# Kernel optimization log

Hardware: AMD Instinct MI355X
Metric: run time of the kernel (lower is better)

Reference implementation:

```python
import jax, jax.numpy as jnp
import numpy as np

MUL0, MUL1 = 128, 64
DIM1 = MUL0 + 3 * MUL1          # 320 = dim of 128x0e + 64x1o
DIM2 = 4                        # 1x0e + 1x1o
WDIM, H = 16, 64
# per-instruction weight sizes (mul_in2 = 1), e3nn instruction order
N1 = MUL0 * MUL0                # (0e x 0e -> 0e)
N2 = MUL0 * MUL1                # (0e x 1o -> 1o)
N3 = MUL1 * MUL1                # (1o x 0e -> 1o)
N4 = MUL1 * MUL0                # (1o x 1o -> 0e)
WNUMEL = N1 + N2 + N3 + N4      # 36864
FAN = MUL0 + MUL1               # summed fan-in per output slice = 192
PW0 = float(np.sqrt(1.0 / FAN))         # path weight, component/element norm, l_out=0
PW1 = float(np.sqrt(3.0 / FAN))         # l_out=1 (alpha = 2l+1 = 3)
INV_SQRT3 = float(1.0 / np.sqrt(3.0))   # wigner_3j(1,1,0)/(0,1,1)/(1,0,1) entries
SQRT_K = float(1.0 / np.sqrt(FAN))      # tp_rescale correction (output divided by this)


def setup_inputs() -> dict:
    key = jax.random.key(0)
    ks = jax.random.split(key, 8)
    N = 4096

    def lin(k, fin, fout):
        k1, k2 = jax.random.split(k)
        lim = 1.0 / np.sqrt(fin)
        W = jax.random.uniform(k1, (fin, fout), minval=-lim, maxval=lim, dtype=jnp.float32)
        b = jax.random.uniform(k2, (fout,), minval=-lim, maxval=lim, dtype=jnp.float32)
        return W, b

    W0, b0 = lin(ks[3], WDIM, H)
    W1, b1 = lin(ks[4], H, H)
    W2, b2 = lin(ks[5], H, WNUMEL)
    return {
        "data_in1": jax.random.normal(ks[0], (N, DIM1), dtype=jnp.float32),
        "data_in2": jax.random.normal(ks[1], (N, DIM2), dtype=jnp.float32),
        "weight": jax.random.normal(ks[2], (N, WDIM), dtype=jnp.float32),
        "W0": W0, "b0": b0, "W1": W1, "b1": b1, "W2": W2, "b2": b2,
        "bias": jax.random.uniform(ks[6], (MUL0,), minval=-SQRT_K, maxval=SQRT_K, dtype=jnp.float32),
    }


def _forward(data_in1, data_in2, weight, W0, b0, W1, b1, W2, b2, bias):
    # weight-generating MLP: 16 -> 64 -> 64 -> weight_numel
    h = jax.nn.relu(weight @ W0 + b0)
    h = jax.nn.relu(h @ W1 + b1)
    w = h @ W2 + b2                                   # [N, WNUMEL] per-sample tp weights
    # split inputs into irrep blocks
    s1 = data_in1[:, :MUL0]                           # [N,128]  128x0e
    v1 = data_in1[:, MUL0:].reshape(-1, MUL1, 3)      # [N,64,3]  64x1o
    s2 = data_in2[:, 0]                               # [N]       1x0e
    v2 = data_in2[:, 1:4]                             # [N,3]     1x1o
    # per-instruction weight views (uvw with v=1 collapsed)
    Wa = w[:, :N1].reshape(-1, MUL0, MUL0)                   # 0e x 0e -> 0e
    Wb = w[:, N1:N1 + N2].reshape(-1, MUL0, MUL1)            # 0e x 1o -> 1o
    Wc = w[:, N1 + N2:N1 + N2 + N3].reshape(-1, MUL1, MUL1)  # 1o x 0e -> 1o
    Wd = w[:, N1 + N2 + N3:].reshape(-1, MUL1, MUL0)         # 1o x 1o -> 0e
    dot12 = jnp.einsum('eui,ei->eu', v1, v2)          # [N,64]
    # scalar (0e) output slice: paths Wa (w3j=1) and Wd (w3j = delta/sqrt(3))
    out0 = PW0 * (jnp.einsum('euw,eu->ew', Wa, s1) * s2[:, None]
                  + INV_SQRT3 * jnp.einsum('euw,eu->ew', Wd, dot12))
    # vector (1o) output slice: paths Wb and Wc (w3j = delta/sqrt(3))
    out1 = PW1 * INV_SQRT3 * (
        jnp.einsum('euw,eu->ew', Wb, s1)[:, :, None] * v2[:, None, :]
        + jnp.einsum('euw,eui->ewi', Wc, v1) * s2[:, None, None])
    out = jnp.concatenate([out0, out1.reshape(-1, 3 * MUL1)], axis=1)  # [N,320]
    out = out / SQRT_K                                # tp_rescale: divide by sqrt_k correction
    out = out.at[:, :MUL0].add(bias)                  # bias added on 0e slice only
    return out


def reference(data_in1, data_in2, weight, W0, b0, W1, b1, W2, b2, bias):
    return _forward(data_in1, data_in2, weight, W0, b0, W1, b1, W2, b2, bias)
```

## Files before the change

### kernel.cpp

```cpp
#include <hip/hip_runtime.h>
#include <hip/hip_bf16.h>

typedef __attribute__((ext_vector_type(8))) short short8;
typedef __attribute__((ext_vector_type(4))) float f32x4;
typedef __attribute__((ext_vector_type(4))) unsigned uint4v;

constexpr int N1 = 16384, N2 = 8192, N3 = 4096;
constexpr int WN = 36864;
constexpr float ISQ3 = 0.57735026918962576451f;

__device__ __forceinline__ unsigned short f2bf(float f) {
  unsigned u = __builtin_bit_cast(unsigned, f);
  u += 0x7fffu + ((u >> 16) & 1u);
  return (unsigned short)(u >> 16);
}

__device__ __forceinline__ unsigned pkbf(float a, float b) {
  unsigned r;
  asm("v_cvt_pk_bf16_f32 %0, %1, %2" : "=v"(r) : "v"(a), "v"(b));
  return r;
}

#define MFMA(a, b, c) __builtin_amdgcn_mfma_f32_16x16x32_bf16((a), (b), (c), 0, 0, 0)

#define CVT8(X0, X1, G) do { uint4v w_;                                       \
    w_[0] = pkbf(X0[0], X0[1]); w_[1] = pkbf(X0[2], X0[3]);                   \
    w_[2] = pkbf(X1[0], X1[1]); w_[3] = pkbf(X1[2], X1[3]);                   \
    G = __builtin_bit_cast(short8, w_); } while (0)

#define LOADH(EF, LO, HI) do {                                                \
    const float* hp_ = H + (size_t)(e0 + 16 * (EF) + nl) * 64 + grp * 8;      \
    f32x4 x0_ = *(const f32x4*)hp_,        x1_ = *(const f32x4*)(hp_ + 4);    \
    f32x4 x2_ = *(const f32x4*)(hp_ + 32), x3_ = *(const f32x4*)(hp_ + 36);   \
    CVT8(x0_, x1_, LO); CVT8(x2_, x3_, HI); } while (0)

__global__ __launch_bounds__(256)
void k_prep(const float* __restrict__ wgt, const float* __restrict__ W0,
            const float* __restrict__ b0, const float* __restrict__ W1,
            const float* __restrict__ b1, const float* __restrict__ W2,
            const float* __restrict__ d1, const float* __restrict__ d2,
            float* __restrict__ H, unsigned short* __restrict__ Bp,
            float* __restrict__ sBg, float* __restrict__ sDg,
            float* __restrict__ sCg, float* __restrict__ d2T) {
  __shared__ __align__(16) float shm[10400];
  const int bid = blockIdx.x;
  const int tid = threadIdx.x;

  if (bid < 288) {
    const int n0 = bid * 128;
#pragma unroll
    for (int q = 0; q < 8; ++q) {
      const int flat = tid + q * 256;
      const int row = flat >> 5, c4 = flat & 31;
      *(f32x4*)&shm[row * 132 + c4 * 4] =
          *(const f32x4*)(W2 + (size_t)row * WN + n0 + c4 * 4);
    }
    __syncthreads();
#pragma unroll
    for (int q = 0; q < 4; ++q) {
      const int p = tid + q * 256;
      const int ntl = p >> 7, kh = (p >> 6) & 1, lane2 = p & 63;
      const int k0 = kh * 32 + (lane2 >> 4) * 8;
      const int col = ntl * 16 + (lane2 & 15);
      short8 v;
#pragma unroll
      for (int qq = 0; qq < 8; ++qq) v[qq] = (short)f2bf(shm[(k0 + qq) * 132 + col]);
      *(short8*)(Bp + ((size_t)(n0 * 8 + p)) * 8) = v;
    }
  } else if (bid < 1312) {
    float* h0s = shm;
    const int r = tid >> 6, jj = tid & 63;
    const int e = (bid - 288) * 4 + r;
    float a = b0[jj];
#pragma unroll
    for (int i = 0; i < 16; ++i) a = fmaf(wgt[e * 16 + i], W0[i * 64 + jj], a);
    h0s[r * 64 + jj] = fmaxf(a, 0.f);
    __syncthreads();
    float a1 = b1[jj];
#pragma unroll
    for (int i = 0; i < 64; ++i) a1 = fmaf(h0s[r * 64 + i], W1[i * 64 + jj], a1);
    H[e * 64 + jj] = fmaxf(a1, 0.f);
  } else {
    float* d1s = shm;
    float* d2s = shm + 10272;
    const int e0 = (bid - 1312) * 32;
    for (int x = tid; x < 32 * 320; x += 256) {
      int e = x / 320, c = x % 320;
      d1s[e * 321 + c] = d1[(size_t)(e0 + e) * 320 + c];
    }
    if (tid < 128) d2s[tid] = d2[(size_t)e0 * 4 + tid];
    __syncthreads();
    const int e = tid & 31;
    const float s2 = d2s[e * 4 + 0];
    const float w1 = d2s[e * 4 + 1], w2 = d2s[e * 4 + 2], w3 = d2s[e * 4 + 3];
    for (int row = 128 + (tid >> 5); row < 516; row += 8) {
      float v; float* dst;
      if (row < 256)      { v = d1s[e * 321 + (row - 128)];            dst = sBg + (size_t)(row - 128) * 4096; }
      else if (row < 320) { int u = row - 256;
        v = ISQ3 * (d1s[e * 321 + 128 + 3 * u] * w1 + d1s[e * 321 + 129 + 3 * u] * w2 +
                    d1s[e * 321 + 130 + 3 * u] * w3);                  dst = sDg + (size_t)u * 4096; }
      else if (row < 512) { v = d1s[e * 321 + 128 + (row - 320)] * s2; dst = sCg + (size_t)(row - 320) * 4096; }
      else                { v = d2s[e * 4 + (row - 512)];              dst = d2T + (size_t)(row - 512) * 4096; }
      dst[e0 + e] = v;
    }
  }
}

__global__ __launch_bounds__(256, 3)
void k_main(const float* __restrict__ sBg, const float* __restrict__ sDg,
            const float* __restrict__ sCg, const float* __restrict__ d2T,
            const float* __restrict__ H, const unsigned short* __restrict__ Bp,
            const float* __restrict__ b2, const float* __restrict__ bias,
            float* __restrict__ out) {
  __shared__ __align__(16) float buf[8448];
  const int bid = blockIdx.x, tid = threadIdx.x;
  const int wid = tid >> 6, lane = tid & 63;
  const int nl = lane & 15, grp = lane >> 4;
  const short8* Bp8 = (const short8*)Bp;
  const f32x4 Zv = {0.f, 0.f, 0.f, 0.f};

  if (bid < 512) {
    const int j = bid & 7;
    const int e0 = (bid >> 3) * 64;
    short8 hL0, hH0, hL1, hH1, hL2, hH2, hL3, hH3;
    LOADH(0, hL0, hH0);
    LOADH(1, hL1, hH1);
    LOADH(2, hL2, hH2);
    LOADH(3, hL3, hH3);

    f32x4 aA0 = Zv, aA1 = Zv, aA2 = Zv, aA3 = Zv;
    f32x4 aD0 = Zv, aD1 = Zv, aD2 = Zv, aD3 = Zv;

    {
      const int u0 = wid * 32;
      const short8* pa = Bp8 + (size_t)(u0 * 8 + j) * 128 + lane;
      const float* sb = sBg + (size_t)u0 * 4096 + e0 + nl;
      const float* pb = b2 + (size_t)u0 * 128 + 16 * j + 4 * grp;
      short8 Fa[3], Fb[3]; f32x4 Bv[3];
      float S0[3], S1[3], S2[3], S3[3];
#pragma unroll
      for (int q = 0; q < 3; ++q) {
        Fa[q] = pa[0]; Fb[q] = pa[64];
        Bv[q] = *(const f32x4*)pb;
        S0[q] = sb[0]; S1[q] = sb[16]; S2[q] = sb[32]; S3[q] = sb[48];
        pa += 1024; sb += 4096; pb += 128;
      }
#pragma unroll
      for (int t = 0; t < 32; ++t) {
        const int s = t % 3;
        short8 f0 = Fa[s], f1 = Fb[s]; f32x4 b = Bv[s];
        float c0 = S0[s], c1 = S1[s], c2 = S2[s], c3 = S3[s];
        if (t < 29) {
          Fa[s] = pa[0]; Fb[s] = pa[64];
          Bv[s] = *(const f32x4*)pb;
          S0[s] = sb[0]; S1[s] = sb[16]; S2[s] = sb[32]; S3[s] = sb[48];
          pa += 1024; sb += 4096; pb += 128;
        }
        f32x4 tt;
        tt = MFMA(f0, hL0, b); tt = MFMA(f1, hH0, tt); aA0 += c0 * tt;
        tt = MFMA(f0, hL1, b); tt = MFMA(f1, hH1, tt); aA1 += c1 * tt;
        tt = MFMA(f0, hL2, b); tt = MFMA(f1, hH2, tt); aA2 += c2 * tt;
        tt = MFMA(f0, hL3, b); tt = MFMA(f1, hH3, tt); aA3 += c3 * tt;
      }
    }
    {
      const int u0 = wid * 16;
      const short8* pa = Bp8 + (size_t)(1792 + u0 * 8 + j) * 128 + lane;
      const float* sd = sDg + (size_t)u0 * 4096 + e0 + nl;
      const float* pb = b2 + (size_t)(N1 + N2 + N3) + (size_t)u0 * 128 + 16 * j + 4 * grp;
      short8 Fa[3], Fb[3]; f32x4 Bv[3];
      float S0[3], S1[3], S2[3], S3[3];
#pragma unroll
      for (int q = 0; q < 3; ++q) {
        Fa[q] = pa[0]; Fb[q] = pa[64];
        Bv[q] = *(const f32x4*)pb;
        S0[q] = sd[0]; S1[q] = sd[16]; S2[q] = sd[32]; S3[q] = sd[48];
        pa += 1024; sd += 4096; pb += 128;
      }
#pragma unroll
      for (int t = 0; t < 16; ++t) {
        const int s = t % 3;
        short8 f0 = Fa[s], f1 = Fb[s]; f32x4 b = Bv[s];
        float c0 = S0[s], c1 = S1[s], c2 = S2[s], c3 = S3[s];
        if (t < 13) {
          Fa[s] = pa[0]; Fb[s] = pa[64];
          Bv[s] = *(const f32x4*)pb;
          S0[s] = sd[0]; S1[s] = sd[16]; S2[s] = sd[32]; S3[s] = sd[48];
          pa += 1024; sd += 4096; pb += 128;
        }
        f32x4 tt;
        tt = MFMA(f0, hL0, b); tt = MFMA(f1, hH0, tt); aD0 += c0 * tt;
        tt = MFMA(f0, hL1, b); tt = MFMA(f1, hH1, tt); aD1 += c1 * tt;
        tt = MFMA(f0, hL2, b); tt = MFMA(f1, hH2, tt); aD2 += c2 * tt;
        tt = MFMA(f0, hL3, b); tt = MFMA(f1, hH3, tt); aD3 += c3 * tt;
      }
    }
    {
      float* bw = &buf[wid * 2112];
#pragma unroll
      for (int r = 0; r < 4; ++r) {
        bw[nl * 33 + grp * 4 + r]             = aA0[r];
        bw[(16 + nl) * 33 + grp * 4 + r]      = aA1[r];
        bw[(32 + nl) * 33 + grp * 4 + r]      = aA2[r];
        bw[(48 + nl) * 33 + grp * 4 + r]      = aA3[r];
        bw[nl * 33 + 16 + grp * 4 + r]        = aD0[r];
        bw[(16 + nl) * 33 + 16 + grp * 4 + r] = aD1[r];
        bw[(32 + nl) * 33 + 16 + grp * 4 + r] = aD2[r];
        bw[(48 + nl) * 33 + 16 + grp * 4 + r] = aD3[r];
      }
      __syncthreads();
#pragma unroll
      for (int it = 0; it < 4; ++it) {
        const int p = tid + it * 256;
        const int e = p >> 4, w = p & 15;
        float ta = buf[e * 33 + w] + buf[2112 + e * 33 + w] +
                   buf[4224 + e * 33 + w] + buf[6336 + e * 33 + w];
        float td = buf[e * 33 + 16 + w] + buf[2112 + e * 33 + 16 + w] +
                   buf[4224 + e * 33 + 16 + w] + buf[6336 + e * 33 + 16 + w];
        out[(size_t)(e0 + e) * 320 + 16 * j + w] = d2T[e0 + e] * ta + td + bias[16 * j + w];
      }
    }
  } else {
    const int idx = bid - 512;
    const int xcd = idx & 7;
    const int jc = xcd & 3;
    const int tile = ((idx >> 3) << 1) | (xcd >> 2);
    const int e0 = tile * 32;
    short8 gL0, gH0, gL1, gH1;
    LOADH(0, gL0, gH0);
    LOADH(1, gL1, gH1);

    f32x4 aB0 = Zv, aB1 = Zv;
    f32x4 c00 = Zv, c01 = Zv, c02 = Zv, c10 = Zv, c11 = Zv, c12 = Zv;

    {
      const int u0 = wid * 32;
      const short8* pa = Bp8 + (size_t)(1024 + u0 * 4 + jc) * 128 + lane;
      const float* sb = sBg + (size_t)u0 * 4096 + e0 + nl;
      const float* pb = b2 + (size_t)N1 + (size_t)u0 * 64 + 16 * jc + 4 * grp;
      short8 Fa[3], Fb[3]; f32x4 Bv[3];
      float S0[3], S1[3];
#pragma unroll
      for (int q = 0; q < 3; ++q) {
        Fa[q] = pa[0]; Fb[q] = pa[64];
        Bv[q] = *(const f32x4*)pb;
        S0[q] = sb[0]; S1[q] = sb[16];
        pa += 512; sb += 4096; pb += 64;
      }
#pragma unroll
      for (int t = 0; t < 32; ++t) {
        const int s = t % 3;
        short8 f0 = Fa[s], f1 = Fb[s]; f32x4 b = Bv[s];
        float c0 = S0[s], c1 = S1[s];
        if (t < 29) {
          Fa[s] = pa[0]; Fb[s] = pa[64];
          Bv[s] = *(const f32x4*)pb;
          S0[s] = sb[0]; S1[s] = sb[16];
          pa += 512; sb += 4096; pb += 64;
        }
        f32x4 tt;
        tt = MFMA(f0, gL0, b); tt = MFMA(f1, gH0, tt); aB0 += c0 * tt;
        tt = MFMA(f0, gL1, b); tt = MFMA(f1, gH1, tt); aB1 += c1 * tt;
      }
    }
    {
      const int u0 = wid * 16;
      const short8* pa = Bp8 + (size_t)(1536 + u0 * 4 + jc) * 128 + lane;
      const float* sc = sCg + (size_t)(3 * u0) * 4096 + e0 + nl;
      const float* pb = b2 + (size_t)(N1 + N2) + (size_t)u0 * 64 + 16 * jc + 4 * grp;
      short8 Fa[3], Fb[3]; f32x4 Bv[3];
      float S00[3], S01[3], S10[3], S11[3], S20[3], S21[3];
#pragma unroll
      for (int q = 0; q < 3; ++q) {
        Fa[q] = pa[0]; Fb[q] = pa[64];
        Bv[q] = *(const f32x4*)pb;
        S00[q] = sc[0]; S01[q] = sc[16];
        S10[q] = sc[4096]; S11[q] = sc[4096 + 16];
        S20[q] = sc[8192]; S21[q] = sc[8192 + 16];
        pa += 512; sc += 12288; pb += 64;
      }
#pragma unroll
      for (int t = 0; t < 16; ++t) {
        const int s = t % 3;
        short8 f0 = Fa[s], f1 = Fb[s]; f32x4 b = Bv[s];
        float d00 = S00[s], d01 = S01[s], d10 = S10[s], d11 = S11[s], d20 = S20[s], d21 = S21[s];
        if (t < 13) {
          Fa[s] = pa[0]; Fb[s] = pa[64];
          Bv[s] = *(const f32x4*)pb;
          S00[s] = sc[0]; S01[s] = sc[16];
          S10[s] = sc[4096]; S11[s] = sc[4096 + 16];
          S20[s] = sc[8192]; S21[s] = sc[8192 + 16];
          pa += 512; sc += 12288; pb += 64;
        }
        f32x4 t0 = MFMA(f0, gL0, b); t0 = MFMA(f1, gH0, t0);
        f32x4 t1 = MFMA(f0, gL1, b); t1 = MFMA(f1, gH1, t1);
        c00 += d00 * t0; c01 += d10 * t0; c02 += d20 * t0;
        c10 += d01 * t1; c11 += d11 * t1; c12 += d21 * t1;
      }
    }
    {
      float* bw = &buf[wid * 2080];
#pragma unroll
      for (int r = 0; r < 4; ++r) {
        const int w1 = grp * 4 + r;
        bw[nl * 65 + w1]             = aB0[r];
        bw[(16 + nl) * 65 + w1]      = aB1[r];
        bw[nl * 65 + 16 + w1]        = c00[r];
        bw[nl * 65 + 32 + w1]        = c01[r];
        bw[nl * 65 + 48 + w1]        = c02[r];
        bw[(16 + nl) * 65 + 16 + w1] = c10[r];
        bw[(16 + nl) * 65 + 32 + w1] = c11[r];
        bw[(16 + nl) * 65 + 48 + w1] = c12[r];
      }
      __syncthreads();
#pragma unroll
      for (int it = 0; it < 6; ++it) {
        const int p = tid + it * 256;
        const int e = p / 48, rem = p % 48;
        const int w1 = rem / 3, i = rem % 3;
        float tb = buf[e * 65 + w1] + buf[2080 + e * 65 + w1] +
                   buf[4160 + e * 65 + w1] + buf[6240 + e * 65 + w1];
        const int co = 16 + i * 16 + w1;
        float tc = buf[e * 65 + co] + buf[2080 + e * 65 + co] +
                   buf[4160 + e * 65 + co] + buf[6240 + e * 65 + co];
        out[(size_t)(e0 + e) * 320 + 128 + (size_t)(16 * jc + w1) * 3 + i] =
            tb * d2T[(1 + i) * 4096 + e0 + e] + tc;
      }
    }
  }
}

extern "C" void kernel_launch(void* const* d_in, const int* in_sizes, int n_in,
                              void* d_out, int out_size, void* d_ws, size_t ws_size,
                              hipStream_t stream) {
  const float* d1   = (const float*)d_in[0];
  const float* d2   = (const float*)d_in[1];
  const float* wgt  = (const float*)d_in[2];
  const float* W0   = (const float*)d_in[3];
  const float* b0   = (const float*)d_in[4];
  const float* W1   = (const float*)d_in[5];
  const float* b1   = (const float*)d_in[6];
  const float* W2   = (const float*)d_in[7];
  const float* b2   = (const float*)d_in[8];
  const float* bias = (const float*)d_in[9];
  float* out = (float*)d_out;

  char* ws = (char*)d_ws;
  float* H           = (float*)(ws);
  unsigned short* Bp = (unsigned short*)(ws + (1u << 20));
  float* sBg         = (float*)(ws + (8u << 20));
  float* sDg         = (float*)(ws + (10u << 20));
  float* sCg         = (float*)(ws + (11u << 20));
  float* d2T         = (float*)(ws + (14u << 20));

  k_prep<<<1440, 256, 0, stream>>>(wgt, W0, b0, W1, b1, W2, d1, d2,
                                   H, Bp, sBg, sDg, sCg, d2T);
  k_main<<<1024, 256, 0, stream>>>(sBg, sDg, sCg, d2T, H, Bp, b2, bias, out);
}
```

Before: 65.07 us.

## Stage weight fragments via global_load_lds ring and cache scalars/bias in LDS

```diff
diff --git a/kernel.cpp b/kernel.cpp
--- a/kernel.cpp
+++ b/kernel.cpp
@@ -4,6 +4,9 @@
 typedef __attribute__((ext_vector_type(8))) short short8;
 typedef __attribute__((ext_vector_type(4))) float f32x4;
 typedef __attribute__((ext_vector_type(4))) unsigned uint4v;
+
+#define GAS __attribute__((address_space(1)))
+#define LAS __attribute__((address_space(3)))
 
 constexpr int N1 = 16384, N2 = 8192, N3 = 4096;
 constexpr int WN = 36864;
@@ -14,14 +17,20 @@
   u += 0x7fffu + ((u >> 16) & 1u);
   return (unsigned short)(u >> 16);
 }
-
 __device__ __forceinline__ unsigned pkbf(float a, float b) {
   unsigned r;
   asm("v_cvt_pk_bf16_f32 %0, %1, %2" : "=v"(r) : "v"(a), "v"(b));
   return r;
 }
+__device__ __forceinline__ float bf2f(unsigned short h) {
+  return __builtin_bit_cast(float, (unsigned)h << 16);
+}
+__device__ __forceinline__ void glds16(const void* g, void* l) {
+  __builtin_amdgcn_global_load_lds((GAS const void*)g, (LAS void*)l, 16, 0, 0);
+}
 
 #define MFMA(a, b, c) __builtin_amdgcn_mfma_f32_16x16x32_bf16((a), (b), (c), 0, 0, 0)
+#define WAITVM(N) asm volatile("s_waitcnt vmcnt(" #N ")" ::: "memory")
 
 #define CVT8(X0, X1, G) do { uint4v w_;                                       \
     w_[0] = pkbf(X0[0], X0[1]); w_[1] = pkbf(X0[2], X0[3]);                   \
@@ -106,97 +115,110 @@
   }
 }
 
-__global__ __launch_bounds__(256, 3)
+__global__ __launch_bounds__(256, 2)
 void k_main(const float* __restrict__ sBg, const float* __restrict__ sDg,
             const float* __restrict__ sCg, const float* __restrict__ d2T,
             const float* __restrict__ H, const unsigned short* __restrict__ Bp,
             const float* __restrict__ b2, const float* __restrict__ bias,
             float* __restrict__ out) {
-  __shared__ __align__(16) float buf[8448];
+  __shared__ __align__(16) char smem[61440];
   const int bid = blockIdx.x, tid = threadIdx.x;
   const int wid = tid >> 6, lane = tid & 63;
   const int nl = lane & 15, grp = lane >> 4;
-  const short8* Bp8 = (const short8*)Bp;
+  const char* BpB = (const char*)Bp;
   const f32x4 Zv = {0.f, 0.f, 0.f, 0.f};
 
   if (bid < 512) {
     const int j = bid & 7;
     const int e0 = (bid >> 3) * 64;
+    {
+      unsigned* dA = (unsigned*)smem;
+      for (int x = tid; x < 4096; x += 256) {
+        const float* s = sBg + (size_t)(x >> 5) * 4096 + e0 + (x & 31) * 2;
+        dA[x] = pkbf(s[0], s[1]);
+      }
+      unsigned* dD = (unsigned*)(smem + 16384);
+      for (int x = tid; x < 2048; x += 256) {
+        const float* s = sDg + (size_t)(x >> 5) * 4096 + e0 + (x & 31) * 2;
+        dD[x] = pkbf(s[0], s[1]);
+      }
+      float* bA = (float*)(smem + 24576);
+      for (int x = tid; x < 2048; x += 256)
+        bA[x] = b2[(size_t)(x >> 4) * 128 + 16 * j + (x & 15)];
+      float* bD = (float*)(smem + 32768);
+      for (int x = tid; x < 1024; x += 256)
+        bD[x] = b2[(size_t)(N1 + N2 + N3) + (size_t)(x >> 4) * 128 + 16 * j + (x & 15)];
+    }
     short8 hL0, hH0, hL1, hH1, hL2, hH2, hL3, hH3;
     LOADH(0, hL0, hH0);
     LOADH(1, hL1, hH1);
     LOADH(2, hL2, hH2);
     LOADH(3, hL3, hH3);
+    __syncthreads();
+
+    const int u0A = wid * 32, u0D = wid * 16;
+    char* ring = smem + 36864 + wid * 6144;
+    const char* gA = BpB + ((size_t)(u0A * 8 + j) * 128 + lane) * 16;
+    const char* gD = BpB + ((size_t)(1792 + u0D * 8 + j) * 128 + lane) * 16;
+    const unsigned short* sbA = (const unsigned short*)smem + (size_t)u0A * 64 + nl;
+    const unsigned short* sdD = (const unsigned short*)(smem + 16384) + (size_t)u0D * 64 + nl;
+    const float* bvA = (const float*)(smem + 24576) + (size_t)u0A * 16 + grp * 4;
+    const float* bvD = (const float*)(smem + 32768) + (size_t)u0D * 16 + grp * 4;
 
     f32x4 aA0 = Zv, aA1 = Zv, aA2 = Zv, aA3 = Zv;
     f32x4 aD0 = Zv, aD1 = Zv, aD2 = Zv, aD3 = Zv;
 
+#define STG_A(K) do { char* dd_ = ring + ((K) % 3) * 2048;                     \
+      glds16(gA + (size_t)(K) * 16384, dd_);                                   \
+      glds16(gA + (size_t)(K) * 16384 + 1024, dd_ + 1024); } while (0)
+#define STG_D(K) do { char* dd_ = ring + ((2 + (K)) % 3) * 2048;               \
+      glds16(gD + (size_t)(K) * 16384, dd_);                                   \
+      glds16(gD + (size_t)(K) * 16384 + 1024, dd_ + 1024); } while (0)
+
+    STG_A(0); STG_A(1);
+#pragma unroll
+    for (int t = 0; t < 32; ++t) {
+      WAITVM(2);
+      if (t < 30) STG_A(t + 2); else STG_D(t - 30);
+      const char* rs = ring + (t % 3) * 2048;
+      short8 f0 = *(const short8*)(rs + lane * 16);
+      short8 f1 = *(const short8*)(rs + 1024 + lane * 16);
+      float c0 = bf2f(sbA[t * 64]);
+      float c1 = bf2f(sbA[t * 64 + 16]);
+      float c2 = bf2f(sbA[t * 64 + 32]);
+      float c3 = bf2f(sbA[t * 64 + 48]);
+      f32x4 bv = *(const f32x4*)(bvA + t * 16);
+      f32x4 tt;
+      tt = MFMA(f0, hL0, bv); tt = MFMA(f1, hH0, tt); aA0 += c0 * tt;
+      tt = MFMA(f0, hL1, bv); tt = MFMA(f1, hH1, tt); aA1 += c1 * tt;
+      tt = MFMA(f0, hL2, bv); tt = MFMA(f1, hH2, tt); aA2 += c2 * tt;
+      tt = MFMA(f0, hL3, bv); tt = MFMA(f1, hH3, tt); aA3 += c3 * tt;
+    }
+#pragma unroll
+    for (int t = 0; t < 16; ++t) {
+      if (t < 14)      { WAITVM(2); STG_D(t + 2); }
+      else if (t == 14){ WAITVM(2); }
+      else             { WAITVM(0); }
+      const char* rs = ring + ((2 + t) % 3) * 2048;
+      short8 f0 = *(const short8*)(rs + lane * 16);
+      short8 f1 = *(const short8*)(rs + 1024 + lane * 16);
+      float c0 = bf2f(sdD[t * 64]);
+      float c1 = bf2f(sdD[t * 64 + 16]);
+      float c2 = bf2f(sdD[t * 64 + 32]);
+      float c3 = bf2f(sdD[t * 64 + 48]);
+      f32x4 bv = *(const f32x4*)(bvD + t * 16);
+      f32x4 tt;
+      tt = MFMA(f0, hL0, bv); tt = MFMA(f1, hH0, tt); aD0 += c0 * tt;
+      tt = MFMA(f0, hL1, bv); tt = MFMA(f1, hH1, tt); aD1 += c1 * tt;
+      tt = MFMA(f0, hL2, bv); tt = MFMA(f1, hH2, tt); aD2 += c2 * tt;
+      tt = MFMA(f0, hL3, bv); tt = MFMA(f1, hH3, tt); aD3 += c3 * tt;
+    }
+#undef STG_A
+#undef STG_D
+    __syncthreads();
+    float* buf = (float*)smem;
     {
-      const int u0 = wid * 32;
-      const short8* pa = Bp8 + (size_t)(u0 * 8 + j) * 128 + lane;
-      const float* sb = sBg + (size_t)u0 * 4096 + e0 + nl;
-      const float* pb = b2 + (size_t)u0 * 128 + 16 * j + 4 * grp;
-      short8 Fa[3], Fb[3]; f32x4 Bv[3];
-      float S0[3], S1[3], S2[3], S3[3];
-#pragma unroll
-      for (int q = 0; q < 3; ++q) {
-        Fa[q] = pa[0]; Fb[q] = pa[64];
-        Bv[q] = *(const f32x4*)pb;
-        S0[q] = sb[0]; S1[q] = sb[16]; S2[q] = sb[32]; S3[q] = sb[48];
-        pa += 1024; sb += 4096; pb += 128;
-      }
-#pragma unroll
-      for (int t = 0; t < 32; ++t) {
-        const int s = t % 3;
-        short8 f0 = Fa[s], f1 = Fb[s]; f32x4 b = Bv[s];
-        float c0 = S0[s], c1 = S1[s], c2 = S2[s], c3 = S3[s];
-        if (t < 29) {
-          Fa[s] = pa[0]; Fb[s] = pa[64];
-          Bv[s] = *(const f32x4*)pb;
-          S0[s] = sb[0]; S1[s] = sb[16]; S2[s] = sb[32]; S3[s] = sb[48];
-          pa += 1024; sb += 4096; pb += 128;
-        }
-        f32x4 tt;
-        tt = MFMA(f0, hL0, b); tt = MFMA(f1, hH0, tt); aA0 += c0 * tt;
-        tt = MFMA(f0, hL1, b); tt = MFMA(f1, hH1, tt); aA1 += c1 * tt;
-        tt = MFMA(f0, hL2, b); tt = MFMA(f1, hH2, tt); aA2 += c2 * tt;
-        tt = MFMA(f0, hL3, b); tt = MFMA(f1, hH3, tt); aA3 += c3 * tt;
-      }
-    }
-    {
-      const int u0 = wid * 16;
-      const short8* pa = Bp8 + (size_t)(1792 + u0 * 8 + j) * 128 + lane;
-      const float* sd = sDg + (size_t)u0 * 4096 + e0 + nl;
-      const float* pb = b2 + (size_t)(N1 + N2 + N3) + (size_t)u0 * 128 + 16 * j + 4 * grp;
-      short8 Fa[3], Fb[3]; f32x4 Bv[3];
-      float S0[3], S1[3], S2[3], S3[3];
-#pragma unroll
-      for (int q = 0; q < 3; ++q) {
-        Fa[q] = pa[0]; Fb[q] = pa[64];
-        Bv[q] = *(const f32x4*)pb;
-        S0[q] = sd[0]; S1[q] = sd[16]; S2[q] = sd[32]; S3[q] = sd[48];
-        pa += 1024; sd += 4096; pb += 128;
-      }
-#pragma unroll
-      for (int t = 0; t < 16; ++t) {
-        const int s = t % 3;
-        short8 f0 = Fa[s], f1 = Fb[s]; f32x4 b = Bv[s];
-        float c0 = S0[s], c1 = S1[s], c2 = S2[s], c3 = S3[s];
-        if (t < 13) {
-          Fa[s] = pa[0]; Fb[s] = pa[64];
-          Bv[s] = *(const f32x4*)pb;
-          S0[s] = sd[0]; S1[s] = sd[16]; S2[s] = sd[32]; S3[s] = sd[48];
-          pa += 1024; sd += 4096; pb += 128;
-        }
-        f32x4 tt;
-        tt = MFMA(f0, hL0, b); tt = MFMA(f1, hH0, tt); aD0 += c0 * tt;
-        tt = MFMA(f0, hL1, b); tt = MFMA(f1, hH1, tt); aD1 += c1 * tt;
-        tt = MFMA(f0, hL2, b); tt = MFMA(f1, hH2, tt); aD2 += c2 * tt;
-        tt = MFMA(f0, hL3, b); tt = MFMA(f1, hH3, tt); aD3 += c3 * tt;
-      }
-    }
-    {
-      float* bw = &buf[wid * 2112];
+      float* bw = buf + wid * 2112;
 #pragma unroll
       for (int r = 0; r < 4; ++r) {
         bw[nl * 33 + grp * 4 + r]             = aA0[r];
@@ -208,17 +230,17 @@
         bw[(32 + nl) * 33 + 16 + grp * 4 + r] = aD2[r];
         bw[(48 + nl) * 33 + 16 + grp * 4 + r] = aD3[r];
       }
-      __syncthreads();
-#pragma unroll
-      for (int it = 0; it < 4; ++it) {
-        const int p = tid + it * 256;
-        const int e = p >> 4, w = p & 15;
-        float ta = buf[e * 33 + w] + buf[2112 + e * 33 + w] +
-                   buf[4224 + e * 33 + w] + buf[6336 + e * 33 + w];
-        float td = buf[e * 33 + 16 + w] + buf[2112 + e * 33 + 16 + w] +
-                   buf[4224 + e * 33 + 16 + w] + buf[6336 + e * 33 + 16 + w];
-        out[(size_t)(e0 + e) * 320 + 16 * j + w] = d2T[e0 + e] * ta + td + bias[16 * j + w];
-      }
+    }
+    __syncthreads();
+#pragma unroll
+    for (int it = 0; it < 4; ++it) {
+      const int p = tid + it * 256;
+      const int e = p >> 4, w = p & 15;
+      float ta = buf[e * 33 + w] + buf[2112 + e * 33 + w] +
+                 buf[4224 + e * 33 + w] + buf[6336 + e * 33 + w];
+      float td = buf[e * 33 + 16 + w] + buf[2112 + e * 33 + 16 + w] +
+                 buf[4224 + e * 33 + 16 + w] + buf[6336 + e * 33 + 16 + w];
+      out[(size_t)(e0 + e) * 320 + 16 * j + w] = d2T[e0 + e] * ta + td + bias[16 * j + w];
     }
   } else {
     const int idx = bid - 512;
@@ -226,80 +248,89 @@
     const int jc = xcd & 3;
     const int tile = ((idx >> 3) << 1) | (xcd >> 2);
     const int e0 = tile * 32;
+    {
+      unsigned* dB = (unsigned*)smem;
+      for (int x = tid; x < 2048; x += 256) {
+        const float* s = sBg + (size_t)(x >> 4) * 4096 + e0 + (x & 15) * 2;
+        dB[x] = pkbf(s[0], s[1]);
+      }
+      unsigned* dC = (unsigned*)(smem + 8192);
+      for (int x = tid; x < 3072; x += 256) {
+        const float* s = sCg + (size_t)(x >> 4) * 4096 + e0 + (x & 15) * 2;
+        dC[x] = pkbf(s[0], s[1]);
+      }
+      float* bB = (float*)(smem + 20480);
+      for (int x = tid; x < 2048; x += 256)
+        bB[x] = b2[(size_t)N1 + (size_t)(x >> 4) * 64 + 16 * jc + (x & 15)];
+      float* bC = (float*)(smem + 28672);
+      for (int x = tid; x < 1024; x += 256)
+        bC[x] = b2[(size_t)(N1 + N2) + (size_t)(x >> 4) * 64 + 16 * jc + (x & 15)];
+    }
     short8 gL0, gH0, gL1, gH1;
     LOADH(0, gL0, gH0);
     LOADH(1, gL1, gH1);
+    __syncthreads();
+
+    const int u0B = wid * 32, u0C = wid * 16;
+    char* ring = smem + 32768 + wid * 6144;
+    const char* gB = BpB + ((size_t)(1024 + u0B * 4 + jc) * 128 + lane) * 16;
+    const char* gC = BpB + ((size_t)(1536 + u0C * 4 + jc) * 128 + lane) * 16;
+    const unsigned short* sbB = (const unsigned short*)smem + (size_t)u0B * 32 + nl;
+    const unsigned short* scC = (const unsigned short*)(smem + 8192) + (size_t)(3 * u0C) * 32 + nl;
+    const float* bvB = (const float*)(smem + 20480) + (size_t)u0B * 16 + grp * 4;
+    const float* bvC = (const float*)(smem + 28672) + (size_t)u0C * 16 + grp * 4;
 
     f32x4 aB0 = Zv, aB1 = Zv;
     f32x4 c00 = Zv, c01 = Zv, c02 = Zv, c10 = Zv, c11 = Zv, c12 = Zv;
 
+#define STG_B(K) do { char* dd_ = ring + ((K) % 3) * 2048;                     \
+      glds16(gB + (size_t)(K) * 8192, dd_);                                    \
+      glds16(gB + (size_t)(K) * 8192 + 1024, dd_ + 1024); } while (0)
+#define STG_C(K) do { char* dd_ = ring + ((2 + (K)) % 3) * 2048;               \
+      glds16(gC + (size_t)(K) * 8192, dd_);                                    \
+      glds16(gC + (size_t)(K) * 8192 + 1024, dd_ + 1024); } while (0)
+
+    STG_B(0); STG_B(1);
+#pragma unroll
+    for (int t = 0; t < 32; ++t) {
+      WAITVM(2);
+      if (t < 30) STG_B(t + 2); else STG_C(t - 30);
+      const char* rs = ring + (t % 3) * 2048;
+      short8 f0 = *(const short8*)(rs + lane * 16);
+      short8 f1 = *(const short8*)(rs + 1024 + lane * 16);
+      float c0 = bf2f(sbB[t * 32]);
+      float c1 = bf2f(sbB[t * 32 + 16]);
+      f32x4 bv = *(const f32x4*)(bvB + t * 16);
+      f32x4 tt;
+      tt = MFMA(f0, gL0, bv); tt = MFMA(f1, gH0, tt); aB0 += c0 * tt;
+      tt = MFMA(f0, gL1, bv); tt = MFMA(f1, gH1, tt); aB1 += c1 * tt;
+    }
+#pragma unroll
+    for (int t = 0; t < 16; ++t) {
+      if (t < 14)      { WAITVM(2); STG_C(t + 2); }
+      else if (t == 14){ WAITVM(2); }
+      else             { WAITVM(0); }
+      const char* rs = ring + ((2 + t) % 3) * 2048;
+      short8 f0 = *(const short8*)(rs + lane * 16);
+      short8 f1 = *(const short8*)(rs + 1024 + lane * 16);
+      float d00 = bf2f(scC[(3 * t) * 32]);
+      float d01 = bf2f(scC[(3 * t) * 32 + 16]);
+      float d10 = bf2f(scC[(3 * t + 1) * 32]);
+      float d11 = bf2f(scC[(3 * t + 1) * 32 + 16]);
+      float d20 = bf2f(scC[(3 * t + 2) * 32]);
+      float d21 = bf2f(scC[(3 * t + 2) * 32 + 16]);
+      f32x4 bv = *(const f32x4*)(bvC + t * 16);
+      f32x4 t0 = MFMA(f0, gL0, bv); t0 = MFMA(f1, gH0, t0);
+      f32x4 t1 = MFMA(f0, gL1, bv); t1 = MFMA(f1, gH1, t1);
+      c00 += d00 * t0; c01 += d10 * t0; c02 += d20 * t0;
+      c10 += d01 * t1; c11 += d11 * t1; c12 += d21 * t1;
+    }
+#undef STG_B
+#undef STG_C
+    __syncthreads();
+    float* buf = (float*)smem;
     {
-      const int u0 = wid * 32;
-      const short8* pa = Bp8 + (size_t)(1024 + u0 * 4 + jc) * 128 + lane;
-      const float* sb = sBg + (size_t)u0 * 4096 + e0 + nl;
-      const float* pb = b2 + (size_t)N1 + (size_t)u0 * 64 + 16 * jc + 4 * grp;
-      short8 Fa[3], Fb[3]; f32x4 Bv[3];
-      float S0[3], S1[3];
-#pragma unroll
-      for (int q = 0; q < 3; ++q) {
-        Fa[q] = pa[0]; Fb[q] = pa[64];
-        Bv[q] = *(const f32x4*)pb;
-        S0[q] = sb[0]; S1[q] = sb[16];
-        pa += 512; sb += 4096; pb += 64;
-      }
-#pragma unroll
-      for (int t = 0; t < 32; ++t) {
-        const int s = t % 3;
-        short8 f0 = Fa[s], f1 = Fb[s]; f32x4 b = Bv[s];
-        float c0 = S0[s], c1 = S1[s];
-        if (t < 29) {
-          Fa[s] = pa[0]; Fb[s] = pa[64];
-          Bv[s] = *(const f32x4*)pb;
-          S0[s] = sb[0]; S1[s] = sb[16];
-          pa += 512; sb += 4096; pb += 64;
-        }
-        f32x4 tt;
-        tt = MFMA(f0, gL0, b); tt = MFMA(f1, gH0, tt); aB0 += c0 * tt;
-        tt = MFMA(f0, gL1, b); tt = MFMA(f1, gH1, tt); aB1 += c1 * tt;
-      }
-    }
-    {
-      const int u0 = wid * 16;
-      const short8* pa = Bp8 + (size_t)(1536 + u0 * 4 + jc) * 128 + lane;
-      const float* sc = sCg + (size_t)(3 * u0) * 4096 + e0 + nl;
-      const float* pb = b2 + (size_t)(N1 + N2) + (size_t)u0 * 64 + 16 * jc + 4 * grp;
-      short8 Fa[3], Fb[3]; f32x4 Bv[3];
-      float S00[3], S01[3], S10[3], S11[3], S20[3], S21[3];
-#pragma unroll
-      for (int q = 0; q < 3; ++q) {
-        Fa[q] = pa[0]; Fb[q] = pa[64];
-        Bv[q] = *(const f32x4*)pb;
-        S00[q] = sc[0]; S01[q] = sc[16];
-        S10[q] = sc[4096]; S11[q] = sc[4096 + 16];
-        S20[q] = sc[8192]; S21[q] = sc[8192 + 16];
-        pa += 512; sc += 12288; pb += 64;
-      }
-#pragma unroll
-      for (int t = 0; t < 16; ++t) {
-        const int s = t % 3;
-        short8 f0 = Fa[s], f1 = Fb[s]; f32x4 b = Bv[s];
-        float d00 = S00[s], d01 = S01[s], d10 = S10[s], d11 = S11[s], d20 = S20[s], d21 = S21[s];
-        if (t < 13) {
-          Fa[s] = pa[0]; Fb[s] = pa[64];
-          Bv[s] = *(const f32x4*)pb;
-          S00[s] = sc[0]; S01[s] = sc[16];
-          S10[s] = sc[4096]; S11[s] = sc[4096 + 16];
-          S20[s] = sc[8192]; S21[s] = sc[8192 + 16];
-          pa += 512; sc += 12288; pb += 64;
-        }
-        f32x4 t0 = MFMA(f0, gL0, b); t0 = MFMA(f1, gH0, t0);
-        f32x4 t1 = MFMA(f0, gL1, b); t1 = MFMA(f1, gH1, t1);
-        c00 += d00 * t0; c01 += d10 * t0; c02 += d20 * t0;
-        c10 += d01 * t1; c11 += d11 * t1; c12 += d21 * t1;
-      }
-    }
-    {
-      float* bw = &buf[wid * 2080];
+      float* bw = buf + wid * 2080;
 #pragma unroll
       for (int r = 0; r < 4; ++r) {
         const int w1 = grp * 4 + r;
@@ -312,20 +343,20 @@
         bw[(16 + nl) * 65 + 32 + w1] = c11[r];
         bw[(16 + nl) * 65 + 48 + w1] = c12[r];
       }
-      __syncthreads();
-#pragma unroll
-      for (int it = 0; it < 6; ++it) {
-        const int p = tid + it * 256;
-        const int e = p / 48, rem = p % 48;
-        const int w1 = rem / 3, i = rem % 3;
-        float tb = buf[e * 65 + w1] + buf[2080 + e * 65 + w1] +
-                   buf[4160 + e * 65 + w1] + buf[6240 + e * 65 + w1];
-        const int co = 16 + i * 16 + w1;
-        float tc = buf[e * 65 + co] + buf[2080 + e * 65 + co] +
-                   buf[4160 + e * 65 + co] + buf[6240 + e * 65 + co];
-        out[(size_t)(e0 + e) * 320 + 128 + (size_t)(16 * jc + w1) * 3 + i] =
-            tb * d2T[(1 + i) * 4096 + e0 + e] + tc;
-      }
+    }
+    __syncthreads();
+#pragma unroll
+    for (int it = 0; it < 6; ++it) {
+      const int p = tid + it * 256;
+      const int e = p / 48, rem = p % 48;
+      const int w1 = rem / 3, i = rem % 3;
+      float tb = buf[e * 65 + w1] + buf[2080 + e * 65 + w1] +
+                 buf[4160 + e * 65 + w1] + buf[6240 + e * 65 + w1];
+      const int co = 16 + i * 16 + w1;
+      float tc = buf[e * 65 + co] + buf[2080 + e * 65 + co] +
+                 buf[4160 + e * 65 + co] + buf[6240 + e * 65 + co];
+      out[(size_t)(e0 + e) * 320 + 128 + (size_t)(16 * jc + w1) * 3 + i] =
+          tb * d2T[(1 + i) * 4096 + e0 + e] + tc;
     }
   }
 }
```

Measured after the change: 72.56 us. 11.5% more time.
